# Optimization experiments

Measured on AMD Instinct MI355X. Metric: run time of the kernel, lower is better.

## Reference

```python
import jax, jax.numpy as jnp
import numpy as np

N_OUT = 4096
N_IN = 4096
TOKENS = 8192
BITWIDTH = 4
GROUP_SIZE = 128
ZERO = 2 ** (BITWIDTH - 1)  # symmetric GPTQ zero-point


def setup_inputs() -> dict:
    key = jax.random.key(0)
    kx, kq, ks = jax.random.split(key, 3)
    x = jax.random.normal(kx, (TOKENS, N_IN), dtype=jnp.float32)
    qweight = jax.random.randint(kq, (N_OUT, N_IN), 0, 2 ** BITWIDTH, dtype=jnp.int32)
    scales = jax.random.uniform(ks, (N_OUT, N_IN // GROUP_SIZE), dtype=jnp.float32) * 0.02 + 0.001
    return {"x": x, "qweight": qweight, "scales": scales}


def reference(x, qweight, scales):
    # Dequantize: W[o, i] = (q[o, i] - zero) * scales[o, i // group_size]
    q = qweight.astype(x.dtype) - jnp.asarray(ZERO, dtype=x.dtype)
    # reshape input dim into (n_groups, group_size) and broadcast group scales
    qg = q.reshape(N_OUT, N_IN // GROUP_SIZE, GROUP_SIZE)
    w = (qg * scales[:, :, None].astype(x.dtype)).reshape(N_OUT, N_IN)
    # out = x @ W^T  -> [tokens, n_out]
    return jnp.einsum('ti,oi->to', x, w)
```

## Files before the change

### kernel.cpp

```cpp
#include <hip/hip_runtime.h>
#include <hip/hip_bf16.h>
#include <stdint.h>

#define TOKENS_C 8192
#define NIN_C    4096
#define NOUT_C   4096
#define GROUP_C  128
#define QZERO_C  8

typedef __bf16 bf16_t;
typedef __bf16  bf16x8 __attribute__((ext_vector_type(8)));
typedef float   f32x4  __attribute__((ext_vector_type(4)));
typedef int     i32x4  __attribute__((ext_vector_type(4)));

#define GAS __attribute__((address_space(1)))
#define LAS __attribute__((address_space(3)))

__device__ __forceinline__ void gload16(const void* g, void* l) {
  __builtin_amdgcn_global_load_lds((const GAS void*)g, (LAS void*)l, 16, 0, 0);
}

__global__ __launch_bounds__(256) void dequant_w_kernel(
    const int* __restrict__ qw, const float* __restrict__ sc,
    bf16_t* __restrict__ wb)
{
  const int t = blockIdx.x * 256 + threadIdx.x;
  const int64_t base = (int64_t)t * 8;
  const int o = (int)(base >> 12);
  const int i = (int)(base & 4095);
  const float s = sc[(o << 5) | (i >> 7)];
  i32x4 q0 = *(const i32x4*)(qw + base);
  i32x4 q1 = *(const i32x4*)(qw + base + 4);
  bf16x8 r;
  r[0] = (bf16_t)((float)(q0[0] - QZERO_C) * s);
  r[1] = (bf16_t)((float)(q0[1] - QZERO_C) * s);
  r[2] = (bf16_t)((float)(q0[2] - QZERO_C) * s);
  r[3] = (bf16_t)((float)(q0[3] - QZERO_C) * s);
  r[4] = (bf16_t)((float)(q1[0] - QZERO_C) * s);
  r[5] = (bf16_t)((float)(q1[1] - QZERO_C) * s);
  r[6] = (bf16_t)((float)(q1[2] - QZERO_C) * s);
  r[7] = (bf16_t)((float)(q1[3] - QZERO_C) * s);
  *(bf16x8*)(wb + base) = r;
}

__global__ __launch_bounds__(256) void cvt_x_kernel(
    const float* __restrict__ x, bf16_t* __restrict__ xb)
{
  const int t = blockIdx.x * 256 + threadIdx.x;
  const int64_t base = (int64_t)t * 8;
  f32x4 a = *(const f32x4*)(x + base);
  f32x4 b = *(const f32x4*)(x + base + 4);
  bf16x8 r;
  r[0] = (bf16_t)a[0]; r[1] = (bf16_t)a[1]; r[2] = (bf16_t)a[2]; r[3] = (bf16_t)a[3];
  r[4] = (bf16_t)b[0]; r[5] = (bf16_t)b[1]; r[6] = (bf16_t)b[2]; r[7] = (bf16_t)b[3];
  *(bf16x8*)(xb + base) = r;
}

#define BM 256
#define BN 256
#define BK 64
#define NT (NIN_C / BK)

__global__ __launch_bounds__(512, 2) void gemm_bt_kernel(
    const bf16_t* __restrict__ A,
    const bf16_t* __restrict__ B,
    float* __restrict__ C)
{
  constexpr int K = NIN_C, N = NOUT_C;
  constexpr int K2 = K * 2;
  __shared__ char smem[131072];

  const int tid  = threadIdx.x;
  const int lane = tid & 63;
  const int wid  = tid >> 6;
  const int wm   = wid >> 2;
  const int wn   = wid & 3;
  const int bm   = blockIdx.x;
  const int bn   = blockIdx.y;

  const int cswz = (((lane & 7) ^ (lane >> 3)) << 4);
  const char* Ag = (const char*)A;
  const char* Bg = (const char*)B;
  int64_t aso[2][2], bso[2][2];
#pragma unroll
  for (int h = 0; h < 2; ++h)
#pragma unroll
    for (int l = 0; l < 2; ++l) {
      const int r = h * 128 + (wid * 2 + l) * 8 + (lane >> 3);
      aso[h][l] = (int64_t)(bm * BM + r) * K2 + cswz;
      bso[h][l] = (int64_t)(bn * BN + r) * K2 + cswz;
    }
  const int sdst = wid * 2048 + (lane << 4);

#define STG_A(tt, h) { char* d_ = smem + (((tt) & 1) << 15) + ((h) << 14) + sdst; \
    gload16(Ag + aso[h][0] + (int64_t)(tt) * 128, d_);                            \
    gload16(Ag + aso[h][1] + (int64_t)(tt) * 128, d_ + 1024); }
#define STG_B(tt, h) { char* d_ = smem + 65536 + (((tt) & 1) << 15) + ((h) << 14) + sdst; \
    gload16(Bg + bso[h][0] + (int64_t)(tt) * 128, d_);                            \
    gload16(Bg + bso[h][1] + (int64_t)(tt) * 128, d_ + 1024); }

  const int frow  = lane & 15;
  const int fcol0 = (((lane >> 4) ^ (lane & 7)) << 4);

#define RD_B(dst, BB, ks)                                                      \
  _Pragma("unroll")                                                            \
  for (int j = 0; j < 4; ++j)                                                  \
    dst[j] = *(const bf16x8*)((BB) + ((wn & 1) * 64 + j * 16 + frow) * 128 +   \
                              (fcol0 ^ ((ks) << 6)));
#define RD_A(AB, mh, ks)                                                       \
  _Pragma("unroll")                                                            \
  for (int i = 0; i < 4; ++i)                                                  \
    a[i] = *(const bf16x8*)((AB) + ((mh) * 64 + i * 16 + frow) * 128 +         \
                            (fcol0 ^ ((ks) << 6)));
#define MM(mh, bv)                                                             \
  __builtin_amdgcn_s_setprio(1);                                               \
  _Pragma("unroll")                                                            \
  for (int i = 0; i < 4; ++i)                                                  \
    _Pragma("unroll")                                                          \
    for (int j = 0; j < 4; ++j)                                                \
      acc[(mh) * 4 + i][j] = __builtin_amdgcn_mfma_f32_16x16x32_bf16(          \
          a[i], bv[j], acc[(mh) * 4 + i][j], 0, 0, 0);                         \
  __builtin_amdgcn_s_setprio(0);
#define BAR __builtin_amdgcn_s_barrier()
#define WAITV(n) asm volatile("s_waitcnt vmcnt(" #n ")" ::: "memory")
#define SBAR0 __builtin_amdgcn_sched_barrier(0)

  const char* Ad0 = smem + wm * 16384;
  const char* Ad1 = smem + 32768 + wm * 16384;
  const char* Bd0 = smem + 65536 + (wn >> 1) * 16384;
  const char* Bd1 = smem + 98304 + (wn >> 1) * 16384;

  f32x4 acc[8][4] = {};
  bf16x8 a[4], b0[4], b1[4];

  STG_A(0, 0); STG_A(0, 1);
  STG_B(0, 0); STG_B(0, 1);
  STG_B(1, 0); STG_B(1, 1);
  WAITV(4);
  BAR; SBAR0;

#define TILE(tt, Ar, Br)                                                       \
   RD_B(b0, Br, 0); RD_A(Ar, 0, 0); STG_A((tt) + 1, 0); MM(0, b0);    \
   RD_A(Ar, 1, 0); STG_A((tt) + 1, 1); MM(1, b0);                     \
   RD_B(b1, Br, 1); RD_A(Ar, 0, 1); MM(0, b1);                        \
  SBAR0; BAR;                                                                  \
   RD_A(Ar, 1, 1); STG_B((tt) + 2, 0); STG_B((tt) + 2, 1);            \
  MM(1, b1); WAITV(4); SBAR0; BAR;

  for (int t0 = 0; t0 < NT - 2; t0 += 2) {
    TILE(t0,     Ad0, Bd0);
    TILE(t0 + 1, Ad1, Bd1);
  }
#undef TILE

  {
    RD_B(b0, Bd0, 0); RD_A(Ad0, 0, 0); STG_A(NT - 1, 0); MM(0, b0);
    RD_A(Ad0, 1, 0); STG_A(NT - 1, 1); MM(1, b0);
    RD_B(b1, Bd0, 1); RD_A(Ad0, 0, 1); MM(0, b1);
    SBAR0; BAR;
    RD_A(Ad0, 1, 1); MM(1, b1); WAITV(0); SBAR0; BAR;
  }
  {
    RD_B(b0, Bd1, 0); RD_A(Ad1, 0, 0); MM(0, b0);
    RD_A(Ad1, 1, 0); MM(1, b0);
    RD_B(b1, Bd1, 1); RD_A(Ad1, 0, 1); MM(0, b1);
    RD_A(Ad1, 1, 1); MM(1, b1);
  }

  const int crow0 = bm * BM + wm * 128;
  const int ccol0 = bn * BN + wn * 64;
  const int r0 = (lane >> 4) << 2;
  const int cc = lane & 15;
#pragma unroll
  for (int fi = 0; fi < 8; ++fi)
#pragma unroll
    for (int j = 0; j < 4; ++j) {
      f32x4 v = acc[fi][j];
#pragma unroll
      for (int r = 0; r < 4; ++r)
        C[(int64_t)(crow0 + fi * 16 + r0 + r) * N + (ccol0 + j * 16 + cc)] = v[r];
    }
#undef STG_A
#undef STG_B
#undef RD_A
#undef RD_B
#undef MM
#undef BAR
#undef WAITV
#undef SBAR0
}

__global__ __launch_bounds__(256) void naive_kernel(
    const float* __restrict__ x, const int* __restrict__ qw,
    const float* __restrict__ sc, float* __restrict__ out)
{
  const int64_t idx = (int64_t)blockIdx.x * 256 + threadIdx.x;
  const int tok = (int)(idx >> 12);
  const int o   = (int)(idx & 4095);
  const float* xr = x + (int64_t)tok * NIN_C;
  const int* qr = qw + (int64_t)o * NIN_C;
  float acc = 0.f;
  for (int g = 0; g < NIN_C / GROUP_C; ++g) {
    float s = sc[(o << 5) | g];
    float ga = 0.f;
#pragma unroll 4
    for (int i = g * GROUP_C; i < (g + 1) * GROUP_C; ++i)
      ga += xr[i] * (float)(qr[i] - QZERO_C);
    acc += s * ga;
  }
  out[idx] = acc;
}

extern "C" void kernel_launch(void* const* d_in, const int* in_sizes, int n_in,
                              void* d_out, int out_size, void* d_ws, size_t ws_size,
                              hipStream_t stream) {
  const float* x  = (const float*)d_in[0];
  const int*   qw = (const int*)d_in[1];
  const float* sc = (const float*)d_in[2];
  float* out = (float*)d_out;

  const size_t xb_bytes = (size_t)TOKENS_C * NIN_C * sizeof(bf16_t);
  const size_t wb_bytes = (size_t)NOUT_C * NIN_C * sizeof(bf16_t);

  if (ws_size < xb_bytes + wb_bytes) {
    const int64_t total = (int64_t)TOKENS_C * NOUT_C;
    naive_kernel<<<(int)(total / 256), 256, 0, stream>>>(x, qw, sc, out);
    return;
  }

  bf16_t* xb = (bf16_t*)d_ws;
  bf16_t* wb = (bf16_t*)((char*)d_ws + xb_bytes);

  {
    const int64_t elems = (int64_t)TOKENS_C * NIN_C;
    cvt_x_kernel<<<(int)(elems / 8 / 256), 256, 0, stream>>>(x, xb);
  }
  {
    const int64_t elems = (int64_t)NOUT_C * NIN_C;
    dequant_w_kernel<<<(int)(elems / 8 / 256), 256, 0, stream>>>(qw, sc, wb);
  }
  {
    dim3 grid(TOKENS_C / BM, NOUT_C / BN);
    gemm_bt_kernel<<<grid, 512, 0, stream>>>(xb, wb, out);
  }
}
```

Baseline: 264.9 us.

## Switch GEMM to int8 MFMA with per-token activation quantization and group scales

Quantizes activations to int8 with a per-token absmax scale and repacks 4-bit weights as signed int8. The GEMM then runs int8 MFMA over each 128-wide group and applies the transposed group scales in fp32 accumulators. It aims to halve operand bandwidth and use the higher int8 matrix throughput. In exchange it adds per-group VALU scale work and loses accuracy from 8-bit activation quantization.

New measurement: 706.9 us. +166.9%, slower.

```diff
diff --git a/kernel.cpp b/kernel.cpp
--- a/kernel.cpp
+++ b/kernel.cpp
@@ -8,8 +8,6 @@
 #define GROUP_C  128
 #define QZERO_C  8
 
-typedef __bf16 bf16_t;
-typedef __bf16  bf16x8 __attribute__((ext_vector_type(8)));
 typedef float   f32x4  __attribute__((ext_vector_type(4)));
 typedef int     i32x4  __attribute__((ext_vector_type(4)));
 
@@ -20,54 +18,74 @@
   __builtin_amdgcn_global_load_lds((const GAS void*)g, (LAS void*)l, 16, 0, 0);
 }
 
-__global__ __launch_bounds__(256) void dequant_w_kernel(
-    const int* __restrict__ qw, const float* __restrict__ sc,
-    bf16_t* __restrict__ wb)
-{
-  const int t = blockIdx.x * 256 + threadIdx.x;
-  const int64_t base = (int64_t)t * 8;
-  const int o = (int)(base >> 12);
-  const int i = (int)(base & 4095);
-  const float s = sc[(o << 5) | (i >> 7)];
-  i32x4 q0 = *(const i32x4*)(qw + base);
-  i32x4 q1 = *(const i32x4*)(qw + base + 4);
-  bf16x8 r;
-  r[0] = (bf16_t)((float)(q0[0] - QZERO_C) * s);
-  r[1] = (bf16_t)((float)(q0[1] - QZERO_C) * s);
-  r[2] = (bf16_t)((float)(q0[2] - QZERO_C) * s);
-  r[3] = (bf16_t)((float)(q0[3] - QZERO_C) * s);
-  r[4] = (bf16_t)((float)(q1[0] - QZERO_C) * s);
-  r[5] = (bf16_t)((float)(q1[1] - QZERO_C) * s);
-  r[6] = (bf16_t)((float)(q1[2] - QZERO_C) * s);
-  r[7] = (bf16_t)((float)(q1[3] - QZERO_C) * s);
-  *(bf16x8*)(wb + base) = r;
-}
-
-__global__ __launch_bounds__(256) void cvt_x_kernel(
-    const float* __restrict__ x, bf16_t* __restrict__ xb)
-{
-  const int t = blockIdx.x * 256 + threadIdx.x;
-  const int64_t base = (int64_t)t * 8;
-  f32x4 a = *(const f32x4*)(x + base);
-  f32x4 b = *(const f32x4*)(x + base + 4);
-  bf16x8 r;
-  r[0] = (bf16_t)a[0]; r[1] = (bf16_t)a[1]; r[2] = (bf16_t)a[2]; r[3] = (bf16_t)a[3];
-  r[4] = (bf16_t)b[0]; r[5] = (bf16_t)b[1]; r[6] = (bf16_t)b[2]; r[7] = (bf16_t)b[3];
-  *(bf16x8*)(xb + base) = r;
+__global__ __launch_bounds__(256) void quant_x_kernel(
+    const float* __restrict__ x, char* __restrict__ x8, float* __restrict__ sx)
+{
+  const int t   = blockIdx.x;
+  const int tid = threadIdx.x;
+  const float* xr = x + (size_t)t * NIN_C;
+  f32x4 v[4];
+#pragma unroll
+  for (int r = 0; r < 4; ++r) v[r] = *(const f32x4*)(xr + tid * 16 + r * 4);
+  float m = 0.f;
+#pragma unroll
+  for (int r = 0; r < 4; ++r)
+#pragma unroll
+    for (int e = 0; e < 4; ++e) m = fmaxf(m, fabsf(v[r][e]));
+#pragma unroll
+  for (int off = 32; off >= 1; off >>= 1) m = fmaxf(m, __shfl_xor(m, off));
+  __shared__ float wmax[4];
+  if ((tid & 63) == 0) wmax[tid >> 6] = m;
+  __syncthreads();
+  m = fmaxf(fmaxf(wmax[0], wmax[1]), fmaxf(wmax[2], wmax[3]));
+  m = fmaxf(m, 1e-20f);
+  const float inv = 127.0f / m;
+  if (tid == 0) sx[t] = m / 127.0f;
+  i32x4 o;
+#pragma unroll
+  for (int r = 0; r < 4; ++r) {
+    int q0 = (int)rintf(v[r][0] * inv), q1 = (int)rintf(v[r][1] * inv);
+    int q2 = (int)rintf(v[r][2] * inv), q3 = (int)rintf(v[r][3] * inv);
+    o[r] = (q0 & 255) | ((q1 & 255) << 8) | ((q2 & 255) << 16) | ((q3 & 255) << 24);
+  }
+  *(i32x4*)(x8 + (size_t)t * NIN_C + tid * 16) = o;
+}
+
+__global__ __launch_bounds__(256) void repack_w_kernel(
+    const int* __restrict__ qw, char* __restrict__ w8)
+{
+  const size_t base = ((size_t)blockIdx.x * 256 + threadIdx.x) * 16;
+  i32x4 o;
+#pragma unroll
+  for (int r = 0; r < 4; ++r) {
+    i32x4 q = *(const i32x4*)(qw + base + r * 4);
+    o[r] = ((q[0] - QZERO_C) & 255) | (((q[1] - QZERO_C) & 255) << 8) |
+           (((q[2] - QZERO_C) & 255) << 16) | (((q[3] - QZERO_C) & 255) << 24);
+  }
+  *(i32x4*)(w8 + base) = o;
+}
+
+__global__ __launch_bounds__(256) void tsc_kernel(
+    const float* __restrict__ sc, float* __restrict__ sT)
+{
+  const int id = blockIdx.x * 256 + threadIdx.x;
+  const int o = id & (NOUT_C - 1), g = id >> 12;
+  sT[id] = sc[o * (NIN_C / GROUP_C) + g];
 }
 
 #define BM 256
 #define BN 256
-#define BK 64
-#define NT (NIN_C / BK)
-
-__global__ __launch_bounds__(512, 2) void gemm_bt_kernel(
-    const bf16_t* __restrict__ A,
-    const bf16_t* __restrict__ B,
+#define BKB 128
+#define NT (NIN_C / BKB)
+
+__global__ __launch_bounds__(512, 2) void gemm_i8_kernel(
+    const char* __restrict__ A,
+    const char* __restrict__ B,
+    const float* __restrict__ sTg,
+    const float* __restrict__ sx,
     float* __restrict__ C)
 {
-  constexpr int K = NIN_C, N = NOUT_C;
-  constexpr int K2 = K * 2;
+  constexpr int N = NOUT_C, KB = NIN_C;
   __shared__ char smem[131072];
 
   const int tid  = threadIdx.x;
@@ -78,113 +96,133 @@
   const int bm   = blockIdx.x;
   const int bn   = blockIdx.y;
 
+  const int frow  = lane & 15;
+  const int klane = lane >> 4;
+  const int swr   = lane & 7;
+
   const int cswz = (((lane & 7) ^ (lane >> 3)) << 4);
-  const char* Ag = (const char*)A;
-  const char* Bg = (const char*)B;
   int64_t aso[2][2], bso[2][2];
 #pragma unroll
   for (int h = 0; h < 2; ++h)
 #pragma unroll
     for (int l = 0; l < 2; ++l) {
       const int r = h * 128 + (wid * 2 + l) * 8 + (lane >> 3);
-      aso[h][l] = (int64_t)(bm * BM + r) * K2 + cswz;
-      bso[h][l] = (int64_t)(bn * BN + r) * K2 + cswz;
+      aso[h][l] = (int64_t)(bm * BM + r) * KB + cswz;
+      bso[h][l] = (int64_t)(bn * BN + r) * KB + cswz;
     }
   const int sdst = wid * 2048 + (lane << 4);
 
 #define STG_A(tt, h) { char* d_ = smem + (((tt) & 1) << 15) + ((h) << 14) + sdst; \
-    gload16(Ag + aso[h][0] + (int64_t)(tt) * 128, d_);                            \
-    gload16(Ag + aso[h][1] + (int64_t)(tt) * 128, d_ + 1024); }
+    gload16(A + aso[h][0] + (tt) * BKB, d_);                                      \
+    gload16(A + aso[h][1] + (tt) * BKB, d_ + 1024); }
 #define STG_B(tt, h) { char* d_ = smem + 65536 + (((tt) & 1) << 15) + ((h) << 14) + sdst; \
-    gload16(Bg + bso[h][0] + (int64_t)(tt) * 128, d_);                            \
-    gload16(Bg + bso[h][1] + (int64_t)(tt) * 128, d_ + 1024); }
-
-  const int frow  = lane & 15;
-  const int fcol0 = (((lane >> 4) ^ (lane & 7)) << 4);
-
-#define RD_B(dst, BB, ks)                                                      \
+    gload16(B + bso[h][0] + (tt) * BKB, d_);                                      \
+    gload16(B + bso[h][1] + (tt) * BKB, d_ + 1024); }
+
+  const int ccol0 = bn * BN + wn * 64;
+
+#define LD_S(dst, g)                                                           \
   _Pragma("unroll")                                                            \
-  for (int j = 0; j < 4; ++j)                                                  \
-    dst[j] = *(const bf16x8*)((BB) + ((wn & 1) * 64 + j * 16 + frow) * 128 +   \
-                              (fcol0 ^ ((ks) << 6)));
-#define RD_A(AB, mh, ks)                                                       \
+  for (int j_ = 0; j_ < 4; ++j_)                                               \
+    dst[j_] = sTg[(size_t)(g) * NOUT_C + ccol0 + j_ * 16 + frow];
+
+#define ARD(Ad, ii, ks) (*(const i32x4*)((Ad) + ((ii) * 16 + frow) * 128 +     \
+                         (((((ks) << 2) | klane) ^ swr) << 4)))
+  i32x4 bf[4][2];
+#define BRD_ALL(Bd)                                                            \
   _Pragma("unroll")                                                            \
-  for (int i = 0; i < 4; ++i)                                                  \
-    a[i] = *(const bf16x8*)((AB) + ((mh) * 64 + i * 16 + frow) * 128 +         \
-                            (fcol0 ^ ((ks) << 6)));
-#define MM(mh, bv)                                                             \
-  __builtin_amdgcn_s_setprio(1);                                               \
-  _Pragma("unroll")                                                            \
-  for (int i = 0; i < 4; ++i)                                                  \
-    _Pragma("unroll")                                                          \
-    for (int j = 0; j < 4; ++j)                                                \
-      acc[(mh) * 4 + i][j] = __builtin_amdgcn_mfma_f32_16x16x32_bf16(          \
-          a[i], bv[j], acc[(mh) * 4 + i][j], 0, 0, 0);                         \
-  __builtin_amdgcn_s_setprio(0);
+  for (int j_ = 0; j_ < 4; ++j_) {                                             \
+    bf[j_][0] = *(const i32x4*)((Bd) + (j_ * 16 + frow) * 128 + ((klane ^ swr) << 4)); \
+    bf[j_][1] = *(const i32x4*)((Bd) + (j_ * 16 + frow) * 128 + (((4 | klane) ^ swr) << 4)); }
+
+  f32x4 facc[8][4] = {};
+  const i32x4 zq = {0, 0, 0, 0};
+
+#define MFI(a_, b_, c_) __builtin_amdgcn_mfma_i32_16x16x64_i8(a_, b_, c_, 0, 0, 0)
+#define SC_APPLY(ii, jj, tv, scur)                                             \
+  { f32x4 tf_;                                                                 \
+    tf_[0] = (float)(tv)[0]; tf_[1] = (float)(tv)[1];                          \
+    tf_[2] = (float)(tv)[2]; tf_[3] = (float)(tv)[3];                          \
+    facc[ii][jj] += tf_ * (scur)[jj]; }
+#define DO_I(ii, Ad, scur)                                                     \
+  { i32x4 ak0_ = ARD(Ad, ii, 0), ak1_ = ARD(Ad, ii, 1);                        \
+    i32x4 t0_, t1_, t2_, t3_;                                                  \
+    __builtin_amdgcn_s_setprio(1);                                             \
+    t0_ = MFI(ak0_, bf[0][0], zq); t0_ = MFI(ak1_, bf[0][1], t0_);             \
+    t1_ = MFI(ak0_, bf[1][0], zq); t1_ = MFI(ak1_, bf[1][1], t1_);             \
+    t2_ = MFI(ak0_, bf[2][0], zq); t2_ = MFI(ak1_, bf[2][1], t2_);             \
+    t3_ = MFI(ak0_, bf[3][0], zq); t3_ = MFI(ak1_, bf[3][1], t3_);             \
+    __builtin_amdgcn_s_setprio(0);                                             \
+    SC_APPLY(ii, 0, t0_, scur); SC_APPLY(ii, 1, t1_, scur);                    \
+    SC_APPLY(ii, 2, t2_, scur); SC_APPLY(ii, 3, t3_, scur); }
+
 #define BAR __builtin_amdgcn_s_barrier()
 #define WAITV(n) asm volatile("s_waitcnt vmcnt(" #n ")" ::: "memory")
 #define SBAR0 __builtin_amdgcn_sched_barrier(0)
 
-  const char* Ad0 = smem + wm * 16384;
-  const char* Ad1 = smem + 32768 + wm * 16384;
-  const char* Bd0 = smem + 65536 + (wn >> 1) * 16384;
-  const char* Bd1 = smem + 98304 + (wn >> 1) * 16384;
-
-  f32x4 acc[8][4] = {};
-  bf16x8 a[4], b0[4], b1[4];
-
+  float sA[4], sB[4];
+
+  LD_S(sA, 0);
+  SBAR0;
   STG_A(0, 0); STG_A(0, 1);
   STG_B(0, 0); STG_B(0, 1);
   STG_B(1, 0); STG_B(1, 1);
   WAITV(4);
   BAR; SBAR0;
 
-#define TILE(tt, Ar, Br)                                                       \
-   RD_B(b0, Br, 0); RD_A(Ar, 0, 0); STG_A((tt) + 1, 0); MM(0, b0);    \
-   RD_A(Ar, 1, 0); STG_A((tt) + 1, 1); MM(1, b0);                     \
-   RD_B(b1, Br, 1); RD_A(Ar, 0, 1); MM(0, b1);                        \
-  SBAR0; BAR;                                                                  \
-   RD_A(Ar, 1, 1); STG_B((tt) + 2, 0); STG_B((tt) + 2, 1);            \
-  MM(1, b1); WAITV(4); SBAR0; BAR;
+#define TILE(tt, par, scur, snxt, DO_SN, DO_SA, DO_SB, WVN)                    \
+  {                                                                            \
+    const char* Ad_ = smem + (par) * 32768 + wm * 16384;                       \
+    const char* Bd_ = smem + 65536 + (par) * 32768 + wn * 8192;                \
+    if (DO_SN) { LD_S(snxt, (tt) + 1); }                                       \
+    BRD_ALL(Bd_);                                                              \
+    if (DO_SA) { STG_A((tt) + 1, 0); }                                         \
+    DO_I(0, Ad_, scur); DO_I(1, Ad_, scur);                                    \
+    if (DO_SA) { STG_A((tt) + 1, 1); }                                         \
+    DO_I(2, Ad_, scur); DO_I(3, Ad_, scur);                                    \
+    DO_I(4, Ad_, scur); DO_I(5, Ad_, scur);                                    \
+    SBAR0; BAR;                                                                \
+    if (DO_SB) { STG_B((tt) + 2, 0); STG_B((tt) + 2, 1); }                     \
+    DO_I(6, Ad_, scur); DO_I(7, Ad_, scur);                                    \
+    WAITV(WVN); SBAR0; BAR;                                                    \
+  }
 
   for (int t0 = 0; t0 < NT - 2; t0 += 2) {
-    TILE(t0,     Ad0, Bd0);
-    TILE(t0 + 1, Ad1, Bd1);
-  }
-#undef TILE
-
+    TILE(t0,     0, sA, sB, 1, 1, 1, 4);
+    TILE(t0 + 1, 1, sB, sA, 1, 1, 1, 4);
+  }
+  TILE(NT - 2, 0, sA, sB, 1, 1, 0, 0);
   {
-    RD_B(b0, Bd0, 0); RD_A(Ad0, 0, 0); STG_A(NT - 1, 0); MM(0, b0);
-    RD_A(Ad0, 1, 0); STG_A(NT - 1, 1); MM(1, b0);
-    RD_B(b1, Bd0, 1); RD_A(Ad0, 0, 1); MM(0, b1);
-    SBAR0; BAR;
-    RD_A(Ad0, 1, 1); MM(1, b1); WAITV(0); SBAR0; BAR;
-  }
-  {
-    RD_B(b0, Bd1, 0); RD_A(Ad1, 0, 0); MM(0, b0);
-    RD_A(Ad1, 1, 0); MM(1, b0);
-    RD_B(b1, Bd1, 1); RD_A(Ad1, 0, 1); MM(0, b1);
-    RD_A(Ad1, 1, 1); MM(1, b1);
+    const char* Ad_ = smem + 32768 + wm * 16384;
+    const char* Bd_ = smem + 65536 + 32768 + wn * 8192;
+    BRD_ALL(Bd_);
+    DO_I(0, Ad_, sB); DO_I(1, Ad_, sB); DO_I(2, Ad_, sB); DO_I(3, Ad_, sB);
+    DO_I(4, Ad_, sB); DO_I(5, Ad_, sB); DO_I(6, Ad_, sB); DO_I(7, Ad_, sB);
   }
 
   const int crow0 = bm * BM + wm * 128;
-  const int ccol0 = bn * BN + wn * 64;
   const int r0 = (lane >> 4) << 2;
-  const int cc = lane & 15;
-#pragma unroll
-  for (int fi = 0; fi < 8; ++fi)
+#pragma unroll
+  for (int fi = 0; fi < 8; ++fi) {
+    const f32x4 sxv = *(const f32x4*)(sx + crow0 + fi * 16 + r0);
 #pragma unroll
     for (int j = 0; j < 4; ++j) {
-      f32x4 v = acc[fi][j];
+      f32x4 v = facc[fi][j];
 #pragma unroll
       for (int r = 0; r < 4; ++r)
-        C[(int64_t)(crow0 + fi * 16 + r0 + r) * N + (ccol0 + j * 16 + cc)] = v[r];
+        C[(int64_t)(crow0 + fi * 16 + r0 + r) * N + (ccol0 + j * 16 + frow)] =
+            v[r] * sxv[r];
     }
+  }
 #undef STG_A
 #undef STG_B
-#undef RD_A
-#undef RD_B
-#undef MM
+#undef LD_S
+#undef ARD
+#undef BRD_ALL
+#undef MFI
+#undef SC_APPLY
+#undef DO_I
+#undef TILE
 #undef BAR
 #undef WAITV
 #undef SBAR0
@@ -219,28 +257,27 @@
   const float* sc = (const float*)d_in[2];
   float* out = (float*)d_out;
 
-  const size_t xb_bytes = (size_t)TOKENS_C * NIN_C * sizeof(bf16_t);
-  const size_t wb_bytes = (size_t)NOUT_C * NIN_C * sizeof(bf16_t);
-
-  if (ws_size < xb_bytes + wb_bytes) {
+  const size_t x8_bytes = (size_t)TOKENS_C * NIN_C;
+  const size_t w8_bytes = (size_t)NOUT_C * NIN_C;
+  const size_t sx_bytes = (size_t)TOKENS_C * sizeof(float);
+  const size_t sT_bytes = (size_t)(NIN_C / GROUP_C) * NOUT_C * sizeof(float);
+
+  if (ws_size < x8_bytes + w8_bytes + sx_bytes + sT_bytes) {
     const int64_t total = (int64_t)TOKENS_C * NOUT_C;
     naive_kernel<<<(int)(total / 256), 256, 0, stream>>>(x, qw, sc, out);
     return;
   }
 
-  bf16_t* xb = (bf16_t*)d_ws;
-  bf16_t* wb = (bf16_t*)((char*)d_ws + xb_bytes);
-
-  {
-    const int64_t elems = (int64_t)TOKENS_C * NIN_C;
-    cvt_x_kernel<<<(int)(elems / 8 / 256), 256, 0, stream>>>(x, xb);
-  }
-  {
-    const int64_t elems = (int64_t)NOUT_C * NIN_C;
-    dequant_w_kernel<<<(int)(elems / 8 / 256), 256, 0, stream>>>(qw, sc, wb);
-  }
+  char*  x8 = (char*)d_ws;
+  char*  w8 = (char*)d_ws + x8_bytes;
+  float* sx = (float*)((char*)d_ws + x8_bytes + w8_bytes);
+  float* sT = (float*)((char*)d_ws + x8_bytes + w8_bytes + sx_bytes);
+
+  quant_x_kernel<<<TOKENS_C, 256, 0, stream>>>(x, x8, sx);
+  repack_w_kernel<<<(int)(w8_bytes / 16 / 256), 256, 0, stream>>>(qw, w8);
+  tsc_kernel<<<(int)((NIN_C / GROUP_C) * NOUT_C / 256), 256, 0, stream>>>(sc, sT);
   {
     dim3 grid(TOKENS_C / BM, NOUT_C / BN);
-    gemm_bt_kernel<<<grid, 512, 0, stream>>>(xb, wb, out);
-  }
-}
+    gemm_i8_kernel<<<grid, 512, 0, stream>>>(x8, w8, sT, sx, out);
+  }
+}
```
